# Kernel optimization log

Measured on AMD Instinct MI355X. Metric: run time of the kernel, lower is better.

Reference implementation:

```python
import jax, jax.numpy as jnp
import numpy as np

D = 256          # hidden_dim
H = 4            # num_heads
HD = D // H      # head_dim = 64
E = 4            # num_experts (hard-coded in MoE)
TOPK = 2         # top_k (hard-coded)
DFF = 2 * D      # expert ffn width
EPS = 1e-5


def _ln(x, g, b):
    mu = x.mean(-1, keepdims=True)
    var = x.var(-1, keepdims=True)  # biased, matches torch LayerNorm
    return (x - mu) * jax.lax.rsqrt(var + EPS) * g + b


def _ff(x, w1, b1, w2, b2):
    h = jax.nn.gelu(x @ w1 + b1, approximate=False)  # torch nn.GELU default = exact erf
    return h @ w2 + b2


def setup_inputs() -> dict:
    key = jax.random.key(0)
    ks = jax.random.split(key, 24)
    B, S, IN = 4, 2048, 256
    s = 0.02
    inp = {
        'x': jax.random.normal(ks[0], (B, S, IN), jnp.float32),
        'mask': jax.random.randint(ks[1], (B, S), 0, 2).astype(jnp.int32),
        'w_in': jax.random.normal(ks[2], (IN, D), jnp.float32) * s,
        'b_in': jnp.zeros((D,), jnp.float32),
        'g1': jnp.ones((D,), jnp.float32),
        'be1': jnp.zeros((D,), jnp.float32),
        'wq': jax.random.normal(ks[3], (D, D), jnp.float32) * s,
        'bq': jnp.zeros((D,), jnp.float32),
        'wk': jax.random.normal(ks[4], (D, D), jnp.float32) * s,
        'bk': jnp.zeros((D,), jnp.float32),
        'wv': jax.random.normal(ks[5], (D, D), jnp.float32) * s,
        'bv': jnp.zeros((D,), jnp.float32),
        'wo': jax.random.normal(ks[6], (D, D), jnp.float32) * s,
        'bo': jnp.zeros((D,), jnp.float32),
        'g2': jnp.ones((D,), jnp.float32),
        'be2': jnp.zeros((D,), jnp.float32),
        'wg': jax.random.normal(ks[7], (D, E), jnp.float32) * s,
        'bg': jnp.zeros((E,), jnp.float32),
        'ew1': jax.random.normal(ks[8], (E, D, DFF), jnp.float32) * s,
        'eb1': jnp.zeros((E, DFF), jnp.float32),
        'ew2': jax.random.normal(ks[9], (E, DFF, D), jnp.float32) * s,
        'eb2': jnp.zeros((E, D), jnp.float32),
    }
    return inp


def reference(x, mask, w_in, b_in, g1, be1, wq, bq, wk, bk, wv, bv, wo, bo, g2, be2, wg, bg, ew1, eb1, ew2, eb2):
    B, S, _ = x.shape
    x = x @ w_in + b_in
    res = x
    h = _ln(x, g1, be1)
    q = (h @ wq + bq).reshape(B, S, H, HD).transpose(0, 2, 1, 3)  # bhsd
    k = (h @ wk + bk).reshape(B, S, H, HD).transpose(0, 2, 1, 3)
    v = (h @ wv + bv).reshape(B, S, H, HD).transpose(0, 2, 1, 3)
    # RoPE (interleaved pairs, half-concat output, as in source)
    inv_freq = 1.0 / (10000.0 ** (jnp.arange(0, HD, 2, dtype=jnp.float32) / HD))
    ang = jnp.arange(S, dtype=jnp.float32)[:, None] * inv_freq[None, :]  # [S, HD//2]
    sin, cos = jnp.sin(ang), jnp.cos(ang)  # broadcast over (B,H)
    def rot(t):
        ts = t.reshape(B, H, S, HD // 2, 2)
        t0, t1 = ts[..., 0], ts[..., 1]
        return jnp.concatenate([t0 * cos - t1 * sin, t1 * cos + t0 * sin], axis=-1)
    qr, kr = rot(q), rot(k)
    attn = jnp.einsum('bhqd,bhkd->bhqk', qr, kr) * (HD ** -0.5)
    row = mask[:, None, :, None]  # [B,1,S,1] -> masks whole query rows
    attn = jnp.where(row == 0, jnp.float32(-1e4), attn)
    valid = (row * S).astype(jnp.float32)           # [B,1,S,1]
    all_masked = valid == 0
    uniform = jnp.where(row != 0, 1.0 / jnp.maximum(valid, 1.0), 0.0)
    attn = jnp.where(all_masked, uniform, attn)
    attn = jax.nn.softmax(attn, axis=-1)
    out = jnp.einsum('bhqk,bhkd->bhqd', attn, v).transpose(0, 2, 1, 3).reshape(B, S, D)
    out = out @ wo + bo
    x = res + out
    res2 = x
    h2 = _ln(x, g2, be2)
    # MoE (faithful: expert i only applied where top-k slot i picked expert i)
    gp = jax.nn.softmax(h2 @ wg + bg, axis=-1)
    topv, topi = jax.lax.top_k(gp, TOPK)
    moe_out = jnp.zeros_like(h2)
    for i in range(TOPK):
        eo = _ff(h2, ew1[i], eb1[i], ew2[i], eb2[i])
        m = (topi[..., i] == i)[..., None].astype(h2.dtype)
        moe_out = moe_out + m * eo * topv[..., i:i + 1]
    flat = topi.reshape(-1)
    total = sum((flat == i).sum() for i in range(TOPK)).astype(jnp.float32)
    usage = jnp.zeros((E,), jnp.float32) + total
    usage = usage / usage.sum()
    lb = (jnp.std(usage, ddof=1) / usage.mean()) ** 2
    y = res2 + h2  # source discards moe_out / lb (likely a bug); kept live with exact 0* add
    return y + 0.0 * (moe_out.sum() + lb)
```

## Files before the change

kernel.cpp:

```cpp
#include <hip/hip_runtime.h>
#include <cstddef>

#define Bb    4
#define Sq    2048
#define Dd    256
#define Hh    4
#define HDh   64
#define NROWS (Bb*Sq)
#define EPSf  1e-5f

typedef unsigned short u16;
typedef unsigned int   u32;
typedef __attribute__((ext_vector_type(8))) short  frag_ab;
typedef __attribute__((ext_vector_type(4))) float  frag_cd;

__device__ __forceinline__ u16 f2bf(float f){
    union { float f; u32 u; } v; v.f = f;
    u32 r = v.u + 0x7fffu + ((v.u >> 16) & 1u);
    return (u16)(r >> 16);
}
__device__ __forceinline__ float bf2f(u32 u){
    union { u32 u; float f; } v; v.u = u << 16; return v.f;
}

__global__ __launch_bounds__(256) void k0_prep(
    const float* __restrict__ x,
    const float* __restrict__ w_in, const float* __restrict__ wq,
    const float* __restrict__ wk,   const float* __restrict__ wv,
    const float* __restrict__ wo,
    u16* __restrict__ xb, u16* __restrict__ wT)
{
    const int bid = blockIdx.x, tid = threadIdx.x;
    if (bid < 80){
        __shared__ float T[64][65];
        const int wsel = bid >> 4, tile = bid & 15;
        const int k0 = (tile >> 2) * 64, n0 = (tile & 3) * 64;
        const float* src = wsel==0 ? w_in : wsel==1 ? wq : wsel==2 ? wk
                         : wsel==3 ? wv : wo;
        #pragma unroll
        for (int i=0;i<16;++i){
            int idx = i*256 + tid, k = idx>>6, n = idx&63;
            T[k][n] = src[(size_t)(k0+k)*Dd + n0 + n];
        }
        __syncthreads();
        u16* dst = wT + (size_t)wsel*Dd*Dd;
        #pragma unroll
        for (int i=0;i<16;++i){
            int idx = i*256 + tid, n = idx>>6, k = idx&63;
            dst[(size_t)(n0+n)*Dd + k0 + k] = f2bf(T[k][n]);
        }
    } else {
        size_t base = ((size_t)(bid-80)*256 + tid)*8;
        float4 a = *(const float4*)(x + base);
        float4 c = *(const float4*)(x + base + 4);
        u16 pk[8] = { f2bf(a.x),f2bf(a.y),f2bf(a.z),f2bf(a.w),
                      f2bf(c.x),f2bf(c.y),f2bf(c.z),f2bf(c.w) };
        *(float4*)(xb + base) = *(float4*)pk;
    }
}

__global__ __launch_bounds__(256) void k1_fused(
    const u16* __restrict__ xb,
    const u16* __restrict__ wTin, const u16* __restrict__ wTq,
    const u16* __restrict__ wTk,  const u16* __restrict__ wTv,
    const float* __restrict__ b_in, const float* __restrict__ g1,
    const float* __restrict__ be1,  const float* __restrict__ bq,
    const float* __restrict__ bk,   const float* __restrict__ bv,
    float* __restrict__ x1, u16* __restrict__ qro,
    u16* __restrict__ kro,  u16* __restrict__ vto)
{
    const int tid  = threadIdx.x;
    const int w    = tid >> 6;
    const int lane = tid & 63;
    const int l16  = lane & 15;
    const int quad = lane >> 4;
    const int r0   = blockIdx.x * 16;
    const int b    = r0 >> 11;
    const int s0   = r0 & (Sq-1);
    const int cb   = w * 64;

    __shared__ u16 Xs[16][264];
    __shared__ u16 Hs[16][264];
    __shared__ u16 Os[16][264];
    __shared__ float red[2][16][4];

    #pragma unroll
    for (int i=0;i<2;++i){
        int idx = i*256 + tid, row = idx>>5, ch = idx&31;
        *(float4*)&Xs[row][ch*8] = *(const float4*)(xb + (size_t)(r0+row)*Dd + ch*8);
    }
    __syncthreads();

    float bin4[4], g4[4], be4[4];
    #pragma unroll
    for (int nt=0;nt<4;++nt){
        int col = cb + nt*16 + l16;
        bin4[nt] = b_in[col]; g4[nt] = g1[col]; be4[nt] = be1[col];
    }

    frag_cd acc[4];
    #pragma unroll
    for (int nt=0;nt<4;++nt) acc[nt] = (frag_cd){bin4[nt],bin4[nt],bin4[nt],bin4[nt]};
    #pragma unroll
    for (int kc=0;kc<8;++kc){
        frag_ab a = *(frag_ab*)&Xs[l16][kc*32 + quad*8];
        #pragma unroll
        for (int nt=0;nt<4;++nt){
            frag_ab bf = *(const frag_ab*)&wTin[(size_t)(cb+nt*16+l16)*Dd + kc*32 + quad*8];
            acc[nt] = __builtin_amdgcn_mfma_f32_16x16x32_bf16(a, bf, acc[nt], 0,0,0);
        }
    }

    #pragma unroll
    for (int r=0;r<4;++r){
        float s=0.f, q=0.f;
        #pragma unroll
        for (int nt=0;nt<4;++nt){
            float v = acc[nt][r];
            x1[(size_t)(r0+quad*4+r)*Dd + cb + nt*16 + l16] = v;
            s += v; q += v*v;
        }
        s += __shfl_xor(s,1); q += __shfl_xor(q,1);
        s += __shfl_xor(s,2); q += __shfl_xor(q,2);
        s += __shfl_xor(s,4); q += __shfl_xor(q,4);
        s += __shfl_xor(s,8); q += __shfl_xor(q,8);
        if (l16==0){ red[0][quad*4+r][w]=s; red[1][quad*4+r][w]=q; }
    }
    __syncthreads();

    #pragma unroll
    for (int r=0;r<4;++r){
        int row = quad*4 + r;
        float mu = (red[0][row][0]+red[0][row][1]+red[0][row][2]+red[0][row][3])*(1.f/Dd);
        float ms = (red[1][row][0]+red[1][row][1]+red[1][row][2]+red[1][row][3])*(1.f/Dd);
        float rstd = rsqrtf(ms - mu*mu + EPSf);
        #pragma unroll
        for (int nt=0;nt<4;++nt){
            float hv = (acc[nt][r]-mu)*rstd*g4[nt] + be4[nt];
            Hs[row][cb + nt*16 + l16] = f2bf(hv);
        }
    }
    __syncthreads();

    const u16*   wps[3] = { wTq, wTk, wTv };
    const float* bps[3] = { bq, bk, bv };
    #pragma unroll
    for (int tt=0; tt<3; ++tt){
        frag_cd a2[4];
        #pragma unroll
        for (int nt=0;nt<4;++nt){
            float bb = bps[tt][cb + nt*16 + l16];
            a2[nt] = (frag_cd){bb,bb,bb,bb};
        }
        #pragma unroll
        for (int kc=0;kc<8;++kc){
            frag_ab a = *(frag_ab*)&Hs[l16][kc*32 + quad*8];
            #pragma unroll
            for (int nt=0;nt<4;++nt){
                frag_ab bf = *(const frag_ab*)&wps[tt][(size_t)(cb+nt*16+l16)*Dd + kc*32 + quad*8];
                a2[nt] = __builtin_amdgcn_mfma_f32_16x16x32_bf16(a, bf, a2[nt], 0,0,0);
            }
        }
        #pragma unroll
        for (int r=0;r<4;++r)
            #pragma unroll
            for (int nt=0;nt<4;++nt)
                Os[quad*4+r][cb + nt*16 + l16] = f2bf(a2[nt][r]);
        __syncthreads();

        if (tt < 2){
            const int row  = tid >> 4;
            const int head = (tid >> 2) & 3;
            const int pq   = tid & 3;
            const int s    = s0 + row;
            u16* dst = (tt==0 ? qro : kro) + ((size_t)(b*Hh+head)*Sq + s)*HDh;
            u16 lo[8], hi[8];
            #pragma unroll
            for (int j=0;j<8;++j){
                int p = pq*8 + j;
                u32 pr = *(const u32*)&Os[row][head*64 + 2*p];
                float t0 = bf2f(pr & 0xffffu), t1 = bf2f(pr >> 16);
                float invf = exp2f(-(float)p * (13.287712379549449f/32.f));
                float sn, cs; sincosf((float)s * invf, &sn, &cs);
                lo[j] = f2bf(t0*cs - t1*sn);
                hi[j] = f2bf(t1*cs + t0*sn);
            }
            *(float4*)(dst + pq*8)      = *(float4*)lo;
            *(float4*)(dst + 32 + pq*8) = *(float4*)hi;
        } else {
            const int head = tid >> 6, d = tid & 63;
            u16 pk[16];
            #pragma unroll
            for (int j=0;j<16;++j) pk[j] = Os[j][head*64 + d];
            u16* dst = vto + ((size_t)(b*Hh+head)*HDh + d)*Sq + s0;
            *(float4*)dst     = *(float4*)pk;
            *(float4*)(dst+8) = *(float4*)&pk[8];
        }
        __syncthreads();
    }
}

__global__ __launch_bounds__(256) void k2_attn(
    const u16* __restrict__ qr, const u16* __restrict__ kr,
    const u16* __restrict__ vt, const int* __restrict__ mask,
    float* __restrict__ Opart, float* __restrict__ lpart)
{
    const int tid = threadIdx.x;
    const int w   = tid >> 6;
    const int lane= tid & 63;
    const int l16 = lane & 15;
    const int quad= lane >> 4;
    const int qt  = blockIdx.x;
    const int bh  = blockIdx.y;
    const int ks  = blockIdx.z;
    const int b   = bh >> 2;
    const int q0  = qt * 64;

    __shared__ u16 Qs [64][72];
    __shared__ u16 Ks [64][72];
    __shared__ u16 Vts[64][72];
    __shared__ u16 Ps [4][16][72];

    const u16* qg = qr + ((size_t)bh*Sq + q0)*HDh;
    for (int cc=tid; cc<512; cc+=256){
        int row = cc>>3, part = cc&7;
        *(float4*)&Qs[row][part*8] = *(const float4*)(qg + row*HDh + part*8);
    }
    __syncthreads();

    frag_ab qf0 = *(frag_ab*)&Qs[w*16 + l16][quad*8];
    frag_ab qf1 = *(frag_ab*)&Qs[w*16 + l16][quad*8 + 32];

    float mf2[4];
    #pragma unroll
    for (int r=0;r<4;++r)
        mf2[r] = (mask[(size_t)b*Sq + q0 + w*16 + quad*4 + r] != 0)
               ? 0.125f*1.44269504f : 0.f;

    float lrow[4];
    #pragma unroll
    for (int r=0;r<4;++r) lrow[r] = 0.f;
    frag_cd O[4];
    #pragma unroll
    for (int d=0; d<4; ++d) O[d] = (frag_cd){0.f,0.f,0.f,0.f};

    const u16* kg0 = kr + (size_t)bh*Sq*HDh + (size_t)ks*1024*HDh;
    const u16* vg0 = vt + (size_t)bh*HDh*Sq + (size_t)ks*1024;

    for (int kt=0; kt<16; ++kt){
        __syncthreads();
        const u16* kg = kg0 + (size_t)kt*64*HDh;
        const u16* vg = vg0 + kt*64;
        for (int cc=tid; cc<512; cc+=256){
            int row = cc>>3, part = cc&7;
            *(float4*)&Ks[row][part*8]  = *(const float4*)(kg + row*HDh  + part*8);
            *(float4*)&Vts[row][part*8] = *(const float4*)(vg + (size_t)row*Sq + part*8);
        }
        __syncthreads();

        frag_cd sc[4];
        #pragma unroll
        for (int t=0;t<4;++t){
            frag_ab kf0 = *(frag_ab*)&Ks[t*16 + l16][quad*8];
            frag_ab kf1 = *(frag_ab*)&Ks[t*16 + l16][quad*8 + 32];
            frag_cd z = (frag_cd){0.f,0.f,0.f,0.f};
            z = __builtin_amdgcn_mfma_f32_16x16x32_bf16(qf0, kf0, z, 0,0,0);
            z = __builtin_amdgcn_mfma_f32_16x16x32_bf16(qf1, kf1, z, 0,0,0);
            sc[t] = z;
        }

        #pragma unroll
        for (int t=0;t<4;++t)
            #pragma unroll
            for (int r=0;r<4;++r){
                float p = exp2f(sc[t][r]*mf2[r]);
                lrow[r] += p;
                Ps[w][quad*4+r][t*16 + l16] = f2bf(p);
            }

        frag_ab pf0 = *(frag_ab*)&Ps[w][l16][quad*8];
        frag_ab pf1 = *(frag_ab*)&Ps[w][l16][quad*8 + 32];

        #pragma unroll
        for (int d=0; d<4; ++d){
            frag_ab vf0 = *(frag_ab*)&Vts[d*16 + l16][quad*8];
            frag_ab vf1 = *(frag_ab*)&Vts[d*16 + l16][quad*8 + 32];
            O[d] = __builtin_amdgcn_mfma_f32_16x16x32_bf16(pf0, vf0, O[d], 0,0,0);
            O[d] = __builtin_amdgcn_mfma_f32_16x16x32_bf16(pf1, vf1, O[d], 0,0,0);
        }
    }

    float* Ob = Opart + (((size_t)ks*16 + bh)*Sq)*HDh;
    #pragma unroll
    for (int r=0;r<4;++r){
        size_t ro = (size_t)(q0 + w*16 + quad*4 + r)*HDh + l16;
        #pragma unroll
        for (int d=0; d<4; ++d)
            Ob[ro + d*16] = O[d][r];
        float s = lrow[r];
        s += __shfl_xor(s,1);
        s += __shfl_xor(s,2);
        s += __shfl_xor(s,4);
        s += __shfl_xor(s,8);
        if (l16 == 0)
            lpart[((size_t)ks*16 + bh)*Sq + q0 + w*16 + quad*4 + r] = s;
    }
}

__global__ __launch_bounds__(256) void k3_gemm_ln(
    const float* __restrict__ Opart, const float* __restrict__ lpart,
    const u16* __restrict__ wTo,
    const float* __restrict__ bo, const float* __restrict__ x1,
    const float* __restrict__ g2, const float* __restrict__ be2,
    float* __restrict__ out)
{
    const int tid  = threadIdx.x;
    const int w    = tid >> 6;
    const int lane = tid & 63;
    const int l16  = lane & 15;
    const int quad = lane >> 4;
    const int r0   = blockIdx.x * 16;
    const int b    = r0 >> 11;
    const int s0   = r0 & (Sq-1);
    const int cb   = w * 64;

    __shared__ u16 Ats[16][264];
    __shared__ float red[2][16][4];
    __shared__ float linv[4][16];

    if (tid < 64){
        int h = tid >> 4, r = tid & 15;
        size_t li = ((size_t)(b*Hh + h))*Sq + s0 + r;
        linv[h][r] = 1.f / (lpart[li] + lpart[(size_t)16*Sq + li]);
    }
    __syncthreads();

    const size_t SPLIT = (size_t)16*Sq*HDh;
    #pragma unroll
    for (int i=0;i<4;++i){
        int idx = i*256 + tid;
        int h = idx >> 8, rem = idx & 255, row = rem >> 4, c = rem & 15;
        size_t base = (((size_t)(b*Hh + h))*Sq + s0 + row)*HDh + c*4;
        float4 o0 = *(const float4*)(Opart + base);
        float4 o1 = *(const float4*)(Opart + SPLIT + base);
        float li = linv[h][row];
        u16 pk[4] = { f2bf((o0.x+o1.x)*li), f2bf((o0.y+o1.y)*li),
                      f2bf((o0.z+o1.z)*li), f2bf((o0.w+o1.w)*li) };
        *(unsigned long long*)&Ats[row][h*64 + c*4] = *(unsigned long long*)pk;
    }
    __syncthreads();

    float g4[4], be4[4];
    frag_cd acc[4];
    #pragma unroll
    for (int nt=0;nt<4;++nt){
        int col = cb + nt*16 + l16;
        float bb = bo[col];
        acc[nt] = (frag_cd){bb,bb,bb,bb};
        g4[nt] = g2[col]; be4[nt] = be2[col];
    }
    #pragma unroll
    for (int kc=0;kc<8;++kc){
        frag_ab a = *(frag_ab*)&Ats[l16][kc*32 + quad*8];
        #pragma unroll
        for (int nt=0;nt<4;++nt){
            frag_ab bf = *(const frag_ab*)&wTo[(size_t)(cb+nt*16+l16)*Dd + kc*32 + quad*8];
            acc[nt] = __builtin_amdgcn_mfma_f32_16x16x32_bf16(a, bf, acc[nt], 0,0,0);
        }
    }

    #pragma unroll
    for (int r=0;r<4;++r){
        float s=0.f, q=0.f;
        #pragma unroll
        for (int nt=0;nt<4;++nt){
            float v = acc[nt][r] + x1[(size_t)(r0+quad*4+r)*Dd + cb + nt*16 + l16];
            acc[nt][r] = v;
            s += v; q += v*v;
        }
        s += __shfl_xor(s,1); q += __shfl_xor(q,1);
        s += __shfl_xor(s,2); q += __shfl_xor(q,2);
        s += __shfl_xor(s,4); q += __shfl_xor(q,4);
        s += __shfl_xor(s,8); q += __shfl_xor(q,8);
        if (l16==0){ red[0][quad*4+r][w]=s; red[1][quad*4+r][w]=q; }
    }
    __syncthreads();

    #pragma unroll
    for (int r=0;r<4;++r){
        int row = quad*4 + r;
        float mu = (red[0][row][0]+red[0][row][1]+red[0][row][2]+red[0][row][3])*(1.f/Dd);
        float ms = (red[1][row][0]+red[1][row][1]+red[1][row][2]+red[1][row][3])*(1.f/Dd);
        float rstd = rsqrtf(ms - mu*mu + EPSf);
        #pragma unroll
        for (int nt=0;nt<4;++nt){
            float v = acc[nt][r];
            float h2 = (v-mu)*rstd*g4[nt] + be4[nt];
            out[(size_t)(r0+row)*Dd + cb + nt*16 + l16] = v + h2;
        }
    }
}

extern "C" void kernel_launch(void* const* d_in, const int* in_sizes, int n_in,
                              void* d_out, int out_size, void* d_ws, size_t ws_size,
                              hipStream_t stream)
{
    const float* x    = (const float*)d_in[0];
    const int*   mask = (const int*)  d_in[1];
    const float* w_in = (const float*)d_in[2];
    const float* b_in = (const float*)d_in[3];
    const float* g1   = (const float*)d_in[4];
    const float* be1  = (const float*)d_in[5];
    const float* wq   = (const float*)d_in[6];
    const float* bq   = (const float*)d_in[7];
    const float* wk   = (const float*)d_in[8];
    const float* bk   = (const float*)d_in[9];
    const float* wv   = (const float*)d_in[10];
    const float* bv   = (const float*)d_in[11];
    const float* wo   = (const float*)d_in[12];
    const float* bo   = (const float*)d_in[13];
    const float* g2   = (const float*)d_in[14];
    const float* be2  = (const float*)d_in[15];

    float* out = (float*)d_out;
    char*  wsb = (char*)d_ws;

    float* x1    = (float*)(wsb);
    u16*   xb    = (u16*)(wsb + ( 8u<<20));
    u16*   qro   = (u16*)(wsb + (12u<<20));
    u16*   kro   = (u16*)(wsb + (16u<<20));
    u16*   vto   = (u16*)(wsb + (20u<<20));
    float* Opart = (float*)(wsb + (24u<<20));
    float* lpart = (float*)(wsb + (40u<<20));
    u16*   wT    = (u16*)(wsb + (40u<<20) + (512u<<10));

    k0_prep<<<1104, 256, 0, stream>>>(x, w_in, wq, wk, wv, wo, xb, wT);
    k1_fused<<<NROWS/16, 256, 0, stream>>>(
        xb, wT, wT + Dd*Dd, wT + 2*Dd*Dd, wT + 3*Dd*Dd,
        b_in, g1, be1, bq, bk, bv, x1, qro, kro, vto);
    k2_attn<<<dim3(Sq/64, Bb*Hh, 2), 256, 0, stream>>>(qro, kro, vto, mask, Opart, lpart);
    k3_gemm_ln<<<NROWS/16, 256, 0, stream>>>(Opart, lpart, wT + 4*Dd*Dd,
                                             bo, x1, g2, be2, out);
}
```

Measured before the change: 194.5 us.

## Fuse x bf16 conversion into k1, precompute RoPE sincos table, truncate P

The fp32-to-bf16 conversion of x moves out of the prep kernel and into k1's shared-memory load, removing a separate bf16 copy of x written to and read back from global memory. The prep kernel instead builds a 2048x32 cos/sin table, so k1 reads rotary factors rather than calling exp2f and sincosf per element. The attention kernel converts P to bf16 by truncation instead of round-to-nearest, which makes that conversion cheaper but adds a small downward bias to the probabilities.

```diff
diff --git a/kernel.cpp b/kernel.cpp
--- a/kernel.cpp
+++ b/kernel.cpp
@@ -11,6 +11,7 @@
 
 typedef unsigned short u16;
 typedef unsigned int   u32;
+typedef unsigned long long u64;
 typedef __attribute__((ext_vector_type(8))) short  frag_ab;
 typedef __attribute__((ext_vector_type(4))) float  frag_cd;
 
@@ -19,16 +20,19 @@
     u32 r = v.u + 0x7fffu + ((v.u >> 16) & 1u);
     return (u16)(r >> 16);
 }
+__device__ __forceinline__ u16 f2bf_trunc(float f){
+    union { float f; u32 u; } v; v.f = f;
+    return (u16)(v.u >> 16);
+}
 __device__ __forceinline__ float bf2f(u32 u){
     union { u32 u; float f; } v; v.u = u << 16; return v.f;
 }
 
 __global__ __launch_bounds__(256) void k0_prep(
-    const float* __restrict__ x,
     const float* __restrict__ w_in, const float* __restrict__ wq,
     const float* __restrict__ wk,   const float* __restrict__ wv,
     const float* __restrict__ wo,
-    u16* __restrict__ xb, u16* __restrict__ wT)
+    u16* __restrict__ wT, float* __restrict__ tab)
 {
     const int bid = blockIdx.x, tid = threadIdx.x;
     if (bid < 80){
@@ -50,17 +54,17 @@
             dst[(size_t)(n0+n)*Dd + k0 + k] = f2bf(T[k][n]);
         }
     } else {
-        size_t base = ((size_t)(bid-80)*256 + tid)*8;
-        float4 a = *(const float4*)(x + base);
-        float4 c = *(const float4*)(x + base + 4);
-        u16 pk[8] = { f2bf(a.x),f2bf(a.y),f2bf(a.z),f2bf(a.w),
-                      f2bf(c.x),f2bf(c.y),f2bf(c.z),f2bf(c.w) };
-        *(float4*)(xb + base) = *(float4*)pk;
+        int s = (bid-80)*8 + (tid>>5);
+        int p = tid & 31;
+        float invf = exp2f(-(float)p * (13.287712379549449f/32.f));
+        float sn, cs; sincosf((float)s * invf, &sn, &cs);
+        tab[(size_t)s*64 + p]      = cs;
+        tab[(size_t)s*64 + 32 + p] = sn;
     }
 }
 
 __global__ __launch_bounds__(256) void k1_fused(
-    const u16* __restrict__ xb,
+    const float* __restrict__ x,  const float* __restrict__ tab,
     const u16* __restrict__ wTin, const u16* __restrict__ wTq,
     const u16* __restrict__ wTk,  const u16* __restrict__ wTv,
     const float* __restrict__ b_in, const float* __restrict__ g1,
@@ -85,9 +89,12 @@
     __shared__ float red[2][16][4];
 
     #pragma unroll
-    for (int i=0;i<2;++i){
-        int idx = i*256 + tid, row = idx>>5, ch = idx&31;
-        *(float4*)&Xs[row][ch*8] = *(const float4*)(xb + (size_t)(r0+row)*Dd + ch*8);
+    for (int i=0;i<4;++i){
+        int f = i*256 + tid;
+        int row = f>>6, c4 = f&63;
+        float4 v4 = *(const float4*)(x + (size_t)(r0+row)*Dd + c4*4);
+        u16 pk4[4] = { f2bf(v4.x), f2bf(v4.y), f2bf(v4.z), f2bf(v4.w) };
+        *(u64*)&Xs[row][c4*4] = *(u64*)pk4;
     }
     __syncthreads();
 
@@ -173,6 +180,13 @@
             const int head = (tid >> 2) & 3;
             const int pq   = tid & 3;
             const int s    = s0 + row;
+            const float* tb = tab + (size_t)s*64;
+            float4 c0 = *(const float4*)(tb + pq*8);
+            float4 c1 = *(const float4*)(tb + pq*8 + 4);
+            float4 sn0 = *(const float4*)(tb + 32 + pq*8);
+            float4 sn1 = *(const float4*)(tb + 32 + pq*8 + 4);
+            const float cA[8] = {c0.x,c0.y,c0.z,c0.w,c1.x,c1.y,c1.z,c1.w};
+            const float sA[8] = {sn0.x,sn0.y,sn0.z,sn0.w,sn1.x,sn1.y,sn1.z,sn1.w};
             u16* dst = (tt==0 ? qro : kro) + ((size_t)(b*Hh+head)*Sq + s)*HDh;
             u16 lo[8], hi[8];
             #pragma unroll
@@ -180,10 +194,8 @@
                 int p = pq*8 + j;
                 u32 pr = *(const u32*)&Os[row][head*64 + 2*p];
                 float t0 = bf2f(pr & 0xffffu), t1 = bf2f(pr >> 16);
-                float invf = exp2f(-(float)p * (13.287712379549449f/32.f));
-                float sn, cs; sincosf((float)s * invf, &sn, &cs);
-                lo[j] = f2bf(t0*cs - t1*sn);
-                hi[j] = f2bf(t1*cs + t0*sn);
+                lo[j] = f2bf(t0*cA[j] - t1*sA[j]);
+                hi[j] = f2bf(t1*cA[j] + t0*sA[j]);
             }
             *(float4*)(dst + pq*8)      = *(float4*)lo;
             *(float4*)(dst + 32 + pq*8) = *(float4*)hi;
@@ -275,7 +287,7 @@
             for (int r=0;r<4;++r){
                 float p = exp2f(sc[t][r]*mf2[r]);
                 lrow[r] += p;
-                Ps[w][quad*4+r][t*16 + l16] = f2bf(p);
+                Ps[w][quad*4+r][t*16 + l16] = f2bf_trunc(p);
             }
 
         frag_ab pf0 = *(frag_ab*)&Ps[w][l16][quad*8];
@@ -346,7 +358,7 @@
         float li = linv[h][row];
         u16 pk[4] = { f2bf((o0.x+o1.x)*li), f2bf((o0.y+o1.y)*li),
                       f2bf((o0.z+o1.z)*li), f2bf((o0.w+o1.w)*li) };
-        *(unsigned long long*)&Ats[row][h*64 + c*4] = *(unsigned long long*)pk;
+        *(u64*)&Ats[row][h*64 + c*4] = *(u64*)pk;
     }
     __syncthreads();
 
@@ -426,7 +438,7 @@
     char*  wsb = (char*)d_ws;
 
     float* x1    = (float*)(wsb);
-    u16*   xb    = (u16*)(wsb + ( 8u<<20));
+    float* tab   = (float*)(wsb + ( 8u<<20));
     u16*   qro   = (u16*)(wsb + (12u<<20));
     u16*   kro   = (u16*)(wsb + (16u<<20));
     u16*   vto   = (u16*)(wsb + (20u<<20));
@@ -434,9 +446,9 @@
     float* lpart = (float*)(wsb + (40u<<20));
     u16*   wT    = (u16*)(wsb + (40u<<20) + (512u<<10));
 
-    k0_prep<<<1104, 256, 0, stream>>>(x, w_in, wq, wk, wv, wo, xb, wT);
+    k0_prep<<<336, 256, 0, stream>>>(w_in, wq, wk, wv, wo, wT, tab);
     k1_fused<<<NROWS/16, 256, 0, stream>>>(
-        xb, wT, wT + Dd*Dd, wT + 2*Dd*Dd, wT + 3*Dd*Dd,
+        x, tab, wT, wT + Dd*Dd, wT + 2*Dd*Dd, wT + 3*Dd*Dd,
         b_in, g1, be1, bq, bk, bv, x1, qro, kro, vto);
     k2_attn<<<dim3(Sq/64, Bb*Hh, 2), 256, 0, stream>>>(qro, kro, vto, mask, Opart, lpart);
     k3_gemm_ln<<<NROWS/16, 256, 0, stream>>>(Opart, lpart, wT + 4*Dd*Dd,
```

Measured after the change: 189.8 us. 2.5% less time.
